# Optimization experiments

Measured on AMD Instinct MI355X. Metric: run time of the kernel, lower is better.

Reference implementation:

```python
import jax, jax.numpy as jnp
import numpy as np

N = 100000      # nodes
E = 1600000     # edges (avg degree 16)
D_IN, D_HID, D_OUT = 128, 64, 32


def setup_inputs() -> dict:
    key = jax.random.key(0)
    ks = jax.random.split(key, 11)
    g = lambda k, shape, fan: jax.random.normal(k, shape, jnp.float32) * (1.0 / np.sqrt(fan))
    return {
        "x": jax.random.normal(ks[0], (N, D_IN), jnp.float32),
        "edges_index": jax.random.randint(ks[1], (2, E), 0, N, dtype=jnp.int64),
        # GATConv layer 1 (heads=1): linear weight, attention vectors a_src/a_dst, bias
        "W1": g(ks[2], (D_IN, D_HID), D_IN),
        "a_src1": g(ks[3], (D_HID,), D_HID),
        "a_dst1": g(ks[4], (D_HID,), D_HID),
        "b1": jnp.zeros((D_HID,), jnp.float32),
        # GATConv layer 2
        "W2": g(ks[5], (D_HID, D_OUT), D_HID),
        "a_src2": g(ks[6], (D_OUT,), D_OUT),
        "a_dst2": g(ks[7], (D_OUT,), D_OUT),
        "b2": jnp.zeros((D_OUT,), jnp.float32),
    }


def _gat_conv(x, src, dst, W, a_src, a_dst, b, n):
    """Single-head PyG GATConv: transform, edge attention, per-dst softmax, scatter-add."""
    h = x @ W                                        # [N, D]
    e = jax.nn.leaky_relu((h @ a_src)[src] + (h @ a_dst)[dst], 0.2)  # [E']
    # segment softmax over edges grouped by destination node
    m = jax.ops.segment_max(e, dst, num_segments=n)  # [N]
    w = jnp.exp(e - m[dst])                          # [E']
    s = jax.ops.segment_sum(w, dst, num_segments=n)  # [N]
    att = w / (s[dst] + 1e-16)                       # [E']
    out = jax.ops.segment_sum(att[:, None] * h[src], dst, num_segments=n)  # [N, D]
    return out + b


def reference(x, edges_index, W1, a_src1, a_dst1, b1, W2, a_src2, a_dst2, b2):
    n = x.shape[0]
    loops = jnp.arange(n, dtype=edges_index.dtype)   # GATConv add_self_loops=True
    src = jnp.concatenate([edges_index[0], loops])
    dst = jnp.concatenate([edges_index[1], loops])
    h = jax.nn.relu(_gat_conv(x, src, dst, W1, a_src1, a_dst1, b1, n))
    # F.dropout with training=False is identity (eval mode)
    out = _gat_conv(h, src, dst, W2, a_src2, a_dst2, b2, n)
    return jax.nn.log_softmax(out, axis=1)
```

## Files before the change

kernel.cpp:

```cpp
#include <hip/hip_runtime.h>
#include <math.h>

#define D_IN 128
#define D_HID 64
#define D_OUT 32
#define CAP 48
#define BSH 8
#define NB 391
#define CAPB 4608
#define CHUNK 2048
#define EPT (CHUNK / 256)
#define NPW 4
#define ESHIFT 5.0f
#define ECLAMP 16.0f

typedef __fp16 half2f __attribute__((ext_vector_type(2)));

__device__ __forceinline__ half2f u2h2(unsigned u) {
    union { unsigned u; half2f h; } c; c.u = u; return c.h;
}
__device__ __forceinline__ unsigned h22u(half2f h) {
    union { half2f h; unsigned u; } c; c.h = h; return c.u;
}
__device__ __forceinline__ unsigned short f2h(float f) {
    union { _Float16 h; unsigned short u; } c; c.h = (_Float16)f; return c.u;
}

#if defined(__has_builtin)
#  if __has_builtin(__builtin_amdgcn_fdot2)
#    define HAVE_FDOT2 1
#  else
#    define HAVE_FDOT2 0
#  endif
#else
#  define HAVE_FDOT2 0
#endif

__device__ __forceinline__ float fdot2f(half2f a, half2f b, float c) {
#if HAVE_FDOT2
    return __builtin_amdgcn_fdot2(a, b, c, false);
#else
    return fmaf((float)a.y, (float)b.y, fmaf((float)a.x, (float)b.x, c));
#endif
}

__device__ __forceinline__ void pair_acc(float wA, float wB, uint2 hA, uint2 hB,
                                         float& a0, float& a1, float& a2, float& a3)
{
    half2f wp = __builtin_amdgcn_cvt_pkrtz(wA, wB);
    a0 = fdot2f(wp, u2h2(__builtin_amdgcn_perm(hB.x, hA.x, 0x05040100u)), a0);
    a1 = fdot2f(wp, u2h2(__builtin_amdgcn_perm(hB.x, hA.x, 0x07060302u)), a1);
    a2 = fdot2f(wp, u2h2(__builtin_amdgcn_perm(hB.y, hA.y, 0x05040100u)), a2);
    a3 = fdot2f(wp, u2h2(__builtin_amdgcn_perm(hB.y, hA.y, 0x07060302u)), a3);
}


__global__ __launch_bounds__(256) void init_kernel(int* __restrict__ cursor)
{
    int i = blockIdx.x * 256 + threadIdx.x;
    if (i < NB) cursor[i] = i * CAPB;
}

__global__ __launch_bounds__(256) void part_kernel(
    const int* __restrict__ esrc, const int* __restrict__ edst,
    unsigned* __restrict__ ebuf, int* __restrict__ cursor, int E, int Et)
{
    __shared__ int hist[NB];
    __shared__ int ofs[NB];
    const int t = threadIdx.x;
    const int base = blockIdx.x * CHUNK;

    for (int b = t; b < NB; b += 256) hist[b] = 0;
    __syncthreads();

    int dreg[EPT], sreg[EPT];
#pragma unroll
    for (int k = 0; k < EPT; ++k) {
        int i = base + k * 256 + t;
        int d = -1, s = 0;
        if (i < Et) {
            d = (i < E) ? edst[i] : (i - E);
            s = (i < E) ? esrc[i] : (i - E);
            atomicAdd(&hist[d >> BSH], 1);
        }
        dreg[k] = d; sreg[k] = s;
    }
    __syncthreads();
    for (int b = t; b < NB; b += 256) {
        int c = hist[b];
        ofs[b] = c ? atomicAdd(&cursor[b], c) : 0;
    }
    __syncthreads();
#pragma unroll
    for (int k = 0; k < EPT; ++k) {
        int d = dreg[k];
        if (d >= 0) {
            int bb = d >> BSH;
            int p = atomicAdd(&ofs[bb], 1);
            if (p < (bb + 1) * CAPB)
                ebuf[p] = ((unsigned)sreg[k] << 8) | (unsigned)(d & 255);
        }
    }
}

__global__ __launch_bounds__(256) void fill_bucket_kernel(
    const unsigned* __restrict__ ebuf, const int* __restrict__ cursor,
    int* __restrict__ cnt, int* __restrict__ csr_pad, int n)
{
    __shared__ __align__(16) int lrow[256 * CAP];
    __shared__ int lcnt[256];
    const int b = blockIdx.x;
    const int t = threadIdx.x;
    lcnt[t] = 0;
    __syncthreads();

    const int end = min(cursor[b], (b + 1) * CAPB);
    for (int i = b * CAPB + t; i < end; i += 256) {
        unsigned v = ebuf[i];
        int dloc = (int)(v & 255u);
        int s    = (int)(v >> 8);
        int slot = atomicAdd(&lcnt[dloc], 1);
        if (slot < CAP) lrow[dloc * CAP + slot] = s;
    }
    __syncthreads();

    {
        int m = min(lcnt[t], CAP);
        int* row = lrow + t * CAP;
        for (int a = 1; a < m; ++a) {
            int key = row[a];
            int p = a - 1;
            while (p >= 0 && row[p] > key) { row[p + 1] = row[p]; --p; }
            row[p + 1] = key;
        }
        for (int a = m; a < CAP; ++a) row[a] = 0;
    }
    __syncthreads();

    const int node0 = b << BSH;
    if (node0 + t < n) cnt[node0 + t] = lcnt[t];

    int4* dst = (int4*)(csr_pad + (size_t)node0 * CAP);
    const int4* src = (const int4*)lrow;
    if (node0 + 256 <= n) {
        for (int i = t; i < 256 * CAP / 4; i += 256) dst[i] = src[i];
    } else {
        const int lim = (n - node0) * CAP / 4;
        for (int i = t; i < lim; i += 256) dst[i] = src[i];
    }
}


template<int K, int NC, int RT, int PAD>
__global__ __launch_bounds__(256) void gemm_alpha_kernel(
    const float* __restrict__ A, const float* __restrict__ W,
    const float* __restrict__ a_src, const float* __restrict__ a_dst,
    unsigned short* __restrict__ C, float* __restrict__ as_,
    float* __restrict__ ad_, int M)
{
    constexpr int TM = 64;
    constexpr int CT = 4;
    constexpr int CG = NC / CT;
    constexpr int KS = K + PAD;
    __shared__ float xs[TM * KS];
    __shared__ float ws[K * NC];
    const int t = threadIdx.x;

    for (int i = t; i < K * NC / 4; i += 256)
        ((float4*)ws)[i] = ((const float4*)W)[i];

    const int base = blockIdx.x * TM;
    for (int i = t; i < TM * K / 4; i += 256) {
        int nloc = i / (K / 4);
        int k4   = i % (K / 4);
        int row  = base + nloc;
        float4 v = make_float4(0.f, 0.f, 0.f, 0.f);
        if (row < M)
            v = *(const float4*)(A + (size_t)row * K + k4 * 4);
        *(float4*)(xs + nloc * KS + k4 * 4) = v;
    }
    __syncthreads();

    const int tx = t % CG, ty = t / CG;
    const int r0 = ty * RT, c0 = tx * CT;
    float acc[RT][CT];
#pragma unroll
    for (int i = 0; i < RT; ++i)
#pragma unroll
        for (int j = 0; j < CT; ++j) acc[i][j] = 0.f;

    for (int k = 0; k < K; k += 4) {
        float4 a[RT];
#pragma unroll
        for (int i = 0; i < RT; ++i)
            a[i] = *(const float4*)(xs + (r0 + i) * KS + k);
#pragma unroll
        for (int kk = 0; kk < 4; ++kk) {
            float4 b = *(const float4*)(ws + (k + kk) * NC + c0);
#pragma unroll
            for (int i = 0; i < RT; ++i) {
                float av = kk == 0 ? a[i].x : kk == 1 ? a[i].y :
                           kk == 2 ? a[i].z : a[i].w;
                acc[i][0] = fmaf(av, b.x, acc[i][0]);
                acc[i][1] = fmaf(av, b.y, acc[i][1]);
                acc[i][2] = fmaf(av, b.z, acc[i][2]);
                acc[i][3] = fmaf(av, b.w, acc[i][3]);
            }
        }
    }

    const float4 asv = *(const float4*)(a_src + c0);
    const float4 adv = *(const float4*)(a_dst + c0);
#pragma unroll
    for (int i = 0; i < RT; ++i) {
        int row = base + r0 + i;
        float ps = acc[i][0] * asv.x + acc[i][1] * asv.y +
                   acc[i][2] * asv.z + acc[i][3] * asv.w;
        float pd = acc[i][0] * adv.x + acc[i][1] * adv.y +
                   acc[i][2] * adv.z + acc[i][3] * adv.w;
#pragma unroll
        for (int o = 1; o < CG; o <<= 1) {
            ps += __shfl_xor(ps, o);
            pd += __shfl_xor(pd, o);
        }
        if (row < M) {
            uint2 cv;
            cv.x = h22u(__builtin_amdgcn_cvt_pkrtz(acc[i][0], acc[i][1]));
            cv.y = h22u(__builtin_amdgcn_cvt_pkrtz(acc[i][2], acc[i][3]));
            *(uint2*)(C + (size_t)row * NC + c0) = cv;
            if (tx == 0) { as_[row] = ps; ad_[row] = pd; }
        }
    }
}

__global__ __launch_bounds__(256) void gat_aggr_fused_kernel(
    const int* __restrict__ cnt, const int* __restrict__ csr_pad,
    const float* __restrict__ as1, const float* __restrict__ ad1,
    const unsigned short* __restrict__ h1, const float* __restrict__ b1,
    const float* __restrict__ W2, const float* __restrict__ a2s,
    const float* __restrict__ a2d, unsigned short* __restrict__ h2,
    float* __restrict__ as2, float* __restrict__ ad2, int n)
{
    __shared__ float rbuf[4][64];
    const int t = threadIdx.x;
    const int wave = t >> 6;
    const int lane = t & 63;
    const int half = lane >> 5, j = lane & 31;

    float w2r[32];
#pragma unroll
    for (int k = 0; k < 32; ++k)
        w2r[k] = W2[(size_t)(half * 32 + k) * D_OUT + j];
    const float a2sj = a2s[j], a2dj = a2d[j];

    const int sub = lane >> 4;
    const int q4 = (lane & 15) * 4;
    const unsigned short* hq = h1 + q4;
    const float4 b1v = *(const float4*)(b1 + q4);

    const int d0 = (blockIdx.x * 4 + wave) * NPW;
    if (d0 >= n) return;

    for (int it = 0; it < NPW; ++it) {
        const int d = d0 + it;
        if (d >= n) break;

        const int   deg = min(cnt[d], CAP);
        const float add = ad1[d];
        int s = csr_pad[(size_t)d * CAP + lane];
        s = (lane < deg) ? s : 0;
        const float araw = as1[s];

        const int i0 = sub;
        int sA = __shfl(s, i0),      sB = __shfl(s, i0 + 4);
        int sC = __shfl(s, i0 + 8),  sD = __shfl(s, i0 + 12);
        uint2 hA = *(const uint2*)(hq + (size_t)sA * 64);
        uint2 hB = *(const uint2*)(hq + (size_t)sB * 64);
        uint2 hC = *(const uint2*)(hq + (size_t)sC * 64);
        uint2 hD = *(const uint2*)(hq + (size_t)sD * 64);
        const bool big = deg > 16;
        int sE = 0, sF = 0, sG = 0, sH = 0;
        uint2 hE, hF, hG, hH;
        if (big) {
            sE = __shfl(s, i0 + 16); sF = __shfl(s, i0 + 20);
            sG = __shfl(s, i0 + 24); sH = __shfl(s, i0 + 28);
            hE = *(const uint2*)(hq + (size_t)sE * 64);
            hF = *(const uint2*)(hq + (size_t)sF * 64);
            hG = *(const uint2*)(hq + (size_t)sG * 64);
            hH = *(const uint2*)(hq + (size_t)sH * 64);
        }

        float ev = araw + add;
        float e = (ev > 0.f) ? ev : 0.2f * ev;
        e = (lane < deg) ? fminf(e, ECLAMP) : -1e30f;
        float w = __expf(e - ESHIFT);
        float ssum = w;

        float a0 = 0.f, a1 = 0.f, a2v = 0.f, a3 = 0.f;
        {
            float wA = __shfl(w, i0),      wB = __shfl(w, i0 + 4);
            float wC = __shfl(w, i0 + 8),  wD = __shfl(w, i0 + 12);
            pair_acc(wA, wB, hA, hB, a0, a1, a2v, a3);
            pair_acc(wC, wD, hC, hD, a0, a1, a2v, a3);
            if (big) {
                float wE = __shfl(w, i0 + 16), wF = __shfl(w, i0 + 20);
                float wG = __shfl(w, i0 + 24), wH = __shfl(w, i0 + 28);
                pair_acc(wE, wF, hE, hF, a0, a1, a2v, a3);
                pair_acc(wG, wH, hG, hH, a0, a1, a2v, a3);
            }
        }
        if (deg > 32) {
            for (int tt = 32; tt < deg; tt += 16) {
                const int i1 = tt + sub;
                float wA = __shfl(w, i1),     wB = __shfl(w, i1 + 4);
                float wC = __shfl(w, i1 + 8), wD = __shfl(w, i1 + 12);
                int   tA = __shfl(s, i1),     tB = __shfl(s, i1 + 4);
                int   tC = __shfl(s, i1 + 8), tD = __shfl(s, i1 + 12);
                uint2 gA = *(const uint2*)(hq + (size_t)tA * 64);
                uint2 gB = *(const uint2*)(hq + (size_t)tB * 64);
                uint2 gC = *(const uint2*)(hq + (size_t)tC * 64);
                uint2 gD = *(const uint2*)(hq + (size_t)tD * 64);
                pair_acc(wA, wB, gA, gB, a0, a1, a2v, a3);
                pair_acc(wC, wD, gC, gD, a0, a1, a2v, a3);
            }
        }

#pragma unroll
        for (int o = 16; o <= 32; o <<= 1) {
            a0 += __shfl_xor(a0, o);  a1 += __shfl_xor(a1, o);
            a2v += __shfl_xor(a2v, o); a3 += __shfl_xor(a3, o);
        }
#pragma unroll
        for (int o = 32; o > 0; o >>= 1) ssum += __shfl_xor(ssum, o);

        const float inv = 1.0f / (ssum + 1e-16f);
        float4 rv;
        rv.x = fmaxf(fmaf(a0, inv, b1v.x), 0.f);
        rv.y = fmaxf(fmaf(a1, inv, b1v.y), 0.f);
        rv.z = fmaxf(fmaf(a2v, inv, b1v.z), 0.f);
        rv.w = fmaxf(fmaf(a3, inv, b1v.w), 0.f);
        if (sub == 0) *(float4*)(&rbuf[wave][q4]) = rv;

        const float* rb = &rbuf[wave][half * 32];
        float acc2 = 0.f;
#pragma unroll
        for (int k4 = 0; k4 < 8; ++k4) {
            float4 r4 = *(const float4*)(rb + k4 * 4);
            acc2 = fmaf(r4.x, w2r[k4 * 4 + 0], acc2);
            acc2 = fmaf(r4.y, w2r[k4 * 4 + 1], acc2);
            acc2 = fmaf(r4.z, w2r[k4 * 4 + 2], acc2);
            acc2 = fmaf(r4.w, w2r[k4 * 4 + 3], acc2);
        }
        acc2 += __shfl_xor(acc2, 32);

        float p1 = acc2 * a2sj, p2 = acc2 * a2dj;
#pragma unroll
        for (int o = 16; o > 0; o >>= 1) {
            p1 += __shfl_xor(p1, o);
            p2 += __shfl_xor(p2, o);
        }
        if (lane < 32) h2[(size_t)d * 32 + j] = f2h(acc2);
        if (lane == 0) { as2[d] = p1; ad2[d] = p2; }
    }
}

__global__ __launch_bounds__(256) void gat_aggr32_lsm_kernel(
    const int* __restrict__ cnt, const int* __restrict__ csr_pad,
    const float* __restrict__ as_, const float* __restrict__ ad_,
    const unsigned short* __restrict__ h, const float* __restrict__ bias,
    float* __restrict__ out, int n)
{
    const int wave = threadIdx.x >> 6;
    const int lane = threadIdx.x & 63;
    const int d0 = (blockIdx.x * 4 + wave) * NPW;
    if (d0 >= n) return;

    const int sub = lane >> 3;
    const int q4 = (lane & 7) * 4;
    const unsigned short* hq = h + q4;
    const float4 bv = *(const float4*)(bias + q4);

    for (int it = 0; it < NPW; ++it) {
        const int d = d0 + it;
        if (d >= n) break;

        const int   deg = min(cnt[d], CAP);
        const float add = ad_[d];
        int s = csr_pad[(size_t)d * CAP + lane];
        s = (lane < deg) ? s : 0;
        const float araw = as_[s];

        const int i0 = sub;
        int sA = __shfl(s, i0),      sB = __shfl(s, i0 + 8);
        uint2 hA = *(const uint2*)(hq + (size_t)sA * 32);
        uint2 hB = *(const uint2*)(hq + (size_t)sB * 32);
        const bool big = deg > 16;
        int sC = 0, sD = 0;
        uint2 hC, hD;
        if (big) {
            sC = __shfl(s, i0 + 16); sD = __shfl(s, i0 + 24);
            hC = *(const uint2*)(hq + (size_t)sC * 32);
            hD = *(const uint2*)(hq + (size_t)sD * 32);
        }

        float ev = araw + add;
        float e = (ev > 0.f) ? ev : 0.2f * ev;
        e = (lane < deg) ? fminf(e, ECLAMP) : -1e30f;
        float w = __expf(e - ESHIFT);
        float ssum = w;

        float a0 = 0.f, a1 = 0.f, a2v = 0.f, a3 = 0.f;
        {
            float wA = __shfl(w, i0), wB = __shfl(w, i0 + 8);
            pair_acc(wA, wB, hA, hB, a0, a1, a2v, a3);
            if (big) {
                float wC = __shfl(w, i0 + 16), wD = __shfl(w, i0 + 24);
                pair_acc(wC, wD, hC, hD, a0, a1, a2v, a3);
            }
        }
        if (deg > 32) {
            for (int tt = 32; tt < deg; tt += 16) {
                const int i1 = tt + sub;
                float wA = __shfl(w, i1); float wB = __shfl(w, i1 + 8);
                int   tA = __shfl(s, i1); int   tB = __shfl(s, i1 + 8);
                uint2 gA = *(const uint2*)(hq + (size_t)tA * 32);
                uint2 gB = *(const uint2*)(hq + (size_t)tB * 32);
                pair_acc(wA, wB, gA, gB, a0, a1, a2v, a3);
            }
        }
#pragma unroll
        for (int o = 8; o <= 32; o <<= 1) {
            a0 += __shfl_xor(a0, o);  a1 += __shfl_xor(a1, o);
            a2v += __shfl_xor(a2v, o); a3 += __shfl_xor(a3, o);
        }
#pragma unroll
        for (int o = 32; o > 0; o >>= 1) ssum += __shfl_xor(ssum, o);

        float inv = 1.0f / (ssum + 1e-16f);
        float r0 = fmaf(a0, inv, bv.x), r1 = fmaf(a1, inv, bv.y);
        float r2 = fmaf(a2v, inv, bv.z), r3 = fmaf(a3, inv, bv.w);

        float mx = fmaxf(fmaxf(r0, r1), fmaxf(r2, r3));
#pragma unroll
        for (int o = 1; o <= 4; o <<= 1) mx = fmaxf(mx, __shfl_xor(mx, o));
        float sm = __expf(r0 - mx) + __expf(r1 - mx) +
                   __expf(r2 - mx) + __expf(r3 - mx);
#pragma unroll
        for (int o = 1; o <= 4; o <<= 1) sm += __shfl_xor(sm, o);
        float lg = mx + __logf(sm);
        if (sub == 0) {
            float4 ov = make_float4(r0 - lg, r1 - lg, r2 - lg, r3 - lg);
            *(float4*)(out + (size_t)d * 32 + q4) = ov;
        }
    }
}

extern "C" void kernel_launch(void* const* d_in, const int* in_sizes, int n_in,
                              void* d_out, int out_size, void* d_ws, size_t ws_size,
                              hipStream_t stream) {
    const float* x    = (const float*)d_in[0];
    const int*   ei   = (const int*)  d_in[1];
    const float* W1   = (const float*)d_in[2];
    const float* av1s = (const float*)d_in[3];
    const float* av1d = (const float*)d_in[4];
    const float* b1   = (const float*)d_in[5];
    const float* W2   = (const float*)d_in[6];
    const float* av2s = (const float*)d_in[7];
    const float* av2d = (const float*)d_in[8];
    const float* b2   = (const float*)d_in[9];
    float* out = (float*)d_out;

    const int N  = in_sizes[0] / D_IN;
    const int E  = in_sizes[1] / 2;
    const int Et = E + N;
    const int* esrc = ei;
    const int* edst = ei + E;

    float* ws = (float*)d_ws;
    size_t off = 0;
    unsigned short* h1f = (unsigned short*)(ws + off); off += (size_t)N * 32;
    unsigned short* h2f_ = (unsigned short*)(ws + off); off += (size_t)N * 16;
    float* as1_ = ws + off;               off += N;
    float* ad1_ = ws + off;               off += N;
    float* as2_ = ws + off;               off += N;
    float* ad2_ = ws + off;               off += N;
    int* cnt    = (int*)(ws + off);       off += N;
    int* csr_pad = (int*)(ws + off);      off += (size_t)N * CAP + 64;
    int* cursor = (int*)(ws + off);       off += NB;
    unsigned* ebuf = (unsigned*)(ws + off); off += (size_t)NB * CAPB;

    const int tiles  = (N + 63) / 64;
    const int aggblk = (N + 4 * NPW - 1) / (4 * NPW);
    const int pblk   = (Et + CHUNK - 1) / CHUNK;

    init_kernel<<<(NB + 255) / 256, 256, 0, stream>>>(cursor);
    part_kernel<<<pblk, 256, 0, stream>>>(esrc, edst, ebuf, cursor, E, Et);
    fill_bucket_kernel<<<NB, 256, 0, stream>>>(ebuf, cursor, cnt, csr_pad, N);

    gemm_alpha_kernel<128, 64, 4, 0><<<tiles, 256, 0, stream>>>(
        x, W1, av1s, av1d, h1f, as1_, ad1_, N);

    gat_aggr_fused_kernel<<<aggblk, 256, 0, stream>>>(
        cnt, csr_pad, as1_, ad1_, h1f, b1,
        W2, av2s, av2d, h2f_, as2_, ad2_, N);

    gat_aggr32_lsm_kernel<<<aggblk, 256, 0, stream>>>(
        cnt, csr_pad, as2_, ad2_, h2f_, b2, out, N);
}
```

Baseline: 319.7 us.

## Sort bucket rows with wave-parallel rank sort and padded LDS rows

The bucket fill kernel moves from 256 to 512 threads. Each row is now sorted by a full 64-lane wave that computes every element's rank through shuffles, replacing the serial per-thread insertion sort. LDS rows are padded to 49 ints to avoid bank conflicts during row-wise access, and the output copy becomes a scalar gather with index division instead of int4 stores. This targets the serial, divergent insertion sort, but adds O(m) shuffles per row and loses the vectorized stores.

Result: no change. 318.6 us (-0.3%).

```diff
diff --git a/kernel.cpp b/kernel.cpp
--- a/kernel.cpp
+++ b/kernel.cpp
@@ -5,6 +5,7 @@
 #define D_HID 64
 #define D_OUT 32
 #define CAP 48
+#define CP 49
 #define BSH 8
 #define NB 391
 #define CAPB 4608
@@ -103,50 +104,52 @@
     }
 }
 
-__global__ __launch_bounds__(256) void fill_bucket_kernel(
+__global__ __launch_bounds__(512) void fill_bucket_kernel(
     const unsigned* __restrict__ ebuf, const int* __restrict__ cursor,
     int* __restrict__ cnt, int* __restrict__ csr_pad, int n)
 {
-    __shared__ __align__(16) int lrow[256 * CAP];
+    __shared__ int lrow[256 * CP];
     __shared__ int lcnt[256];
     const int b = blockIdx.x;
     const int t = threadIdx.x;
-    lcnt[t] = 0;
+    if (t < 256) lcnt[t] = 0;
     __syncthreads();
 
     const int end = min(cursor[b], (b + 1) * CAPB);
-    for (int i = b * CAPB + t; i < end; i += 256) {
+    for (int i = b * CAPB + t; i < end; i += 512) {
         unsigned v = ebuf[i];
         int dloc = (int)(v & 255u);
         int s    = (int)(v >> 8);
         int slot = atomicAdd(&lcnt[dloc], 1);
-        if (slot < CAP) lrow[dloc * CAP + slot] = s;
+        if (slot < CAP) lrow[dloc * CP + slot] = s;
     }
     __syncthreads();
 
     {
-        int m = min(lcnt[t], CAP);
-        int* row = lrow + t * CAP;
-        for (int a = 1; a < m; ++a) {
-            int key = row[a];
-            int p = a - 1;
-            while (p >= 0 && row[p] > key) { row[p + 1] = row[p]; --p; }
-            row[p + 1] = key;
-        }
-        for (int a = m; a < CAP; ++a) row[a] = 0;
+        const int wave = t >> 6, lane = t & 63;
+        for (int r = wave; r < 256; r += 8) {
+            const int m = min(lcnt[r], CAP);
+            int v = (lane < m) ? lrow[r * CP + lane] : 0;
+            int rank = 0;
+            for (int j = 0; j < m; ++j) {
+                int vj = __shfl(v, j);
+                rank += (vj < v) || (vj == v && j < lane);
+            }
+            if (lane < m) lrow[r * CP + rank] = v;
+            else if (lane < CAP) lrow[r * CP + lane] = 0;
+        }
     }
     __syncthreads();
 
     const int node0 = b << BSH;
-    if (node0 + t < n) cnt[node0 + t] = lcnt[t];
-
-    int4* dst = (int4*)(csr_pad + (size_t)node0 * CAP);
-    const int4* src = (const int4*)lrow;
-    if (node0 + 256 <= n) {
-        for (int i = t; i < 256 * CAP / 4; i += 256) dst[i] = src[i];
-    } else {
-        const int lim = (n - node0) * CAP / 4;
-        for (int i = t; i < lim; i += 256) dst[i] = src[i];
+    if (t < 256 && node0 + t < n) cnt[node0 + t] = lcnt[t];
+
+    const int rows = min(256, n - node0);
+    const int total = rows * CAP;
+    int* dst = csr_pad + (size_t)node0 * CAP;
+    for (int g = t; g < total; g += 512) {
+        int r = g / CAP, c = g - r * CAP;
+        dst[g] = lrow[r * CP + c];
     }
 }
 
@@ -495,7 +498,7 @@
 
     init_kernel<<<(NB + 255) / 256, 256, 0, stream>>>(cursor);
     part_kernel<<<pblk, 256, 0, stream>>>(esrc, edst, ebuf, cursor, E, Et);
-    fill_bucket_kernel<<<NB, 256, 0, stream>>>(ebuf, cursor, cnt, csr_pad, N);
+    fill_bucket_kernel<<<NB, 512, 0, stream>>>(ebuf, cursor, cnt, csr_pad, N);
 
     gemm_alpha_kernel<128, 64, 4, 0><<<tiles, 256, 0, stream>>>(
         x, W1, av1s, av1d, h1f, as1_, ad1_, N);
```
